# Kernel tuning notes

Measured on AMD Instinct MI355X. Metric: run time of the kernel, lower is better.

The kernel has to match this reference:

```python
import jax, jax.numpy as jnp
import numpy as np

ND, NL, E, M = 8000, 16000, 60000, 50000  # disease nodes, lncrna nodes, edges, label edges
H = 16  # attention heads


def _gat(h_src, h_dst, src, dst, Ws, Wd, a_s, a_d, b, n_dst):
    # PyG GATConv: bipartite, concat heads, add_self_loops=False, negative_slope=0.2
    Hh, C = a_s.shape
    zs = (h_src @ Ws).reshape(-1, Hh, C)   # [Ns,H,C]
    zd = (h_dst @ Wd).reshape(-1, Hh, C)   # [Nd,H,C]
    al = (zs * a_s).sum(-1)[src] + (zd * a_d).sum(-1)[dst]  # [E,H]
    al = jax.nn.leaky_relu(al, negative_slope=0.2)
    m = jax.ops.segment_max(al, dst, num_segments=n_dst)
    m = jnp.where(jnp.isfinite(m), m, 0.0)  # guard empty segments
    e = jnp.exp(al - m[dst])
    s = jax.ops.segment_sum(e, dst, num_segments=n_dst)
    alpha = e / (s[dst] + 1e-16)            # softmax over incoming edges per dst
    msg = zs[src] * alpha[:, :, None]       # [E,H,C]
    out = jax.ops.segment_sum(msg, dst, num_segments=n_dst)
    return out.reshape(n_dst, Hh * C) + b


def _head_mean(x):
    x = jax.nn.relu(x)
    return x.reshape(x.shape[0], H, -1).mean(axis=1)


def _forward(x_d, x_l, emb_d, emb_l, lin_dw, lin_db, lin_lw, lin_lb,
             Wsrc1, Wdst1, asrc1, adst1, b1,
             Wsrc2, Wdst2, asrc2, adst2, b2,
             Wsrc3, Wdst3, asrc3, adst3, b3,
             pw, pb, fc1w, fc1b, fc2w, fc2b,
             node_id_d, node_id_l, edge_src, edge_dst, label_src, label_dst):
    hd = x_d @ lin_dw + lin_db + emb_d[node_id_d]   # [ND,128]
    hl = x_l @ lin_lw + lin_lb + emb_l[node_id_l]   # [NL,128]
    for (Ws, Wd, a_s, a_d, b) in ((Wsrc1, Wdst1, asrc1, adst1, b1),
                                  (Wsrc2, Wdst2, asrc2, adst2, b2),
                                  (Wsrc3, Wdst3, asrc3, adst3, b3)):
        # to_hetero: edge-type 0 = disease->lncrna (target lncrna); 1 = reverse
        out_l = _gat(hd, hl, edge_src, edge_dst, Ws[0], Wd[0], a_s[0], a_d[0], b[0], NL)
        out_d = _gat(hl, hd, edge_dst, edge_src, Ws[1], Wd[1], a_s[1], a_d[1], b[1], ND)
        hd, hl = _head_mean(out_d), _head_mean(out_l)
    # penalty scaling (per node type after to_hetero); transformer branch is dead code
    hd = hd * jnp.exp(hd @ pw[0] + pb[0])
    hl = hl * jnp.exp(hl @ pw[1] + pb[1])
    f = jnp.concatenate([hd[label_src], hl[label_dst]], axis=-1)  # [M,64]
    return jax.nn.relu(f @ fc1w + fc1b) @ fc2w + fc2b              # [M,1]


def setup_inputs():
    key = jax.random.key(0)
    ks = jax.random.split(key, 40)
    def rn(i, shape, scale=1.0):
        return jax.random.normal(ks[i], shape, dtype=jnp.float32) * scale
    return dict(
        x_d=rn(0, (ND, 412)), x_l=rn(1, (NL, 240)),
        node_id_d=jnp.arange(ND), node_id_l=jnp.arange(NL),
        edge_src=jax.random.randint(ks[2], (E,), 0, ND),
        edge_dst=jax.random.randint(ks[3], (E,), 0, NL),
        label_src=jax.random.randint(ks[4], (M,), 0, ND),
        label_dst=jax.random.randint(ks[5], (M,), 0, NL),
        emb_d=rn(6, (ND, 128), 0.1), emb_l=rn(7, (NL, 128), 0.1),
        lin_dw=rn(8, (412, 128), 412 ** -0.5), lin_db=rn(9, (128,), 0.02),
        lin_lw=rn(10, (240, 128), 240 ** -0.5), lin_lb=rn(11, (128,), 0.02),
        Wsrc1=rn(12, (2, 128, 2048), 128 ** -0.5), Wdst1=rn(13, (2, 128, 2048), 128 ** -0.5),
        asrc1=rn(14, (2, H, 128), 0.05), adst1=rn(15, (2, H, 128), 0.05), b1=rn(16, (2, 2048), 0.02),
        Wsrc2=rn(17, (2, 128, 2048), 128 ** -0.5), Wdst2=rn(18, (2, 128, 2048), 128 ** -0.5),
        asrc2=rn(19, (2, H, 128), 0.05), adst2=rn(20, (2, H, 128), 0.05), b2=rn(21, (2, 2048), 0.02),
        Wsrc3=rn(22, (2, 128, 512), 128 ** -0.5), Wdst3=rn(23, (2, 128, 512), 128 ** -0.5),
        asrc3=rn(24, (2, H, 32), 0.05), adst3=rn(25, (2, H, 32), 0.05), b3=rn(26, (2, 512), 0.02),
        pw=rn(27, (2, 32, 1), 0.05), pb=rn(28, (2, 1), 0.01),
        fc1w=rn(29, (64, 64), 64 ** -0.5), fc1b=rn(30, (64,), 0.02),
        fc2w=rn(31, (64, 1), 64 ** -0.5), fc2b=rn(32, (1,), 0.02),
    )


def reference(x_d, x_l, node_id_d, node_id_l, edge_src, edge_dst, label_src, label_dst,
              emb_d, emb_l, lin_dw, lin_db, lin_lw, lin_lb,
              Wsrc1, Wdst1, asrc1, adst1, b1,
              Wsrc2, Wdst2, asrc2, adst2, b2,
              Wsrc3, Wdst3, asrc3, adst3, b3,
              pw, pb, fc1w, fc1b, fc2w, fc2b):
    return _forward(x_d, x_l, emb_d, emb_l, lin_dw, lin_db, lin_lw, lin_lb,
                    Wsrc1, Wdst1, asrc1, adst1, b1,
                    Wsrc2, Wdst2, asrc2, adst2, b2,
                    Wsrc3, Wdst3, asrc3, adst3, b3,
                    pw, pb, fc1w, fc1b, fc2w, fc2b,
                    node_id_d, node_id_l, edge_src, edge_dst, label_src, label_dst)
```

## Files before the change

kernel.cpp:

```cpp
#include <hip/hip_runtime.h>
#include <cstdint>
#include <cstddef>

#define ND 8000
#define NL 16000
#define NE 60000
#define NM 50000

#define BM 64
#define BN 64
#define BK 16

typedef __attribute__((ext_vector_type(8))) short bf16x8;
typedef __attribute__((ext_vector_type(4))) float f32x4;
typedef __attribute__((ext_vector_type(8))) unsigned int u32x8;

__device__ __forceinline__ unsigned short f2bf(float x) {
    unsigned int u = __float_as_uint(x);
    unsigned int r = (u + 0x7FFFu + ((u >> 16) & 1u)) >> 16;
    return (unsigned short)r;
}
__device__ __forceinline__ float bf2f(unsigned short b) {
    return __uint_as_float(((unsigned int)b) << 16);
}
__device__ __forceinline__ float lrelu(float x) {
    return x >= 0.f ? x : 0.2f * x;
}

__device__ __forceinline__ void gl_lds16(const void* g, void* l) {
    __builtin_amdgcn_global_load_lds(
        (const __attribute__((address_space(1))) void*)g,
        (__attribute__((address_space(3))) void*)l, 16, 0, 0);
}

__global__ __launch_bounds__(256) void inlin_kernel(
    const float* __restrict__ x_d, const float* __restrict__ x_l,
    const float* __restrict__ wd, const float* __restrict__ wl,
    const float* __restrict__ bd, const float* __restrict__ bl,
    const float* __restrict__ embd, const float* __restrict__ embl,
    const int* __restrict__ nidd, const int* __restrict__ nidl,
    float* __restrict__ hd, float* __restrict__ hl)
{
    __shared__ float As[BK][32 + 4];
    __shared__ float Bs[BK][BN + 4];
    int mt = blockIdx.y;
    const float* A; const float* B; const float* bias; const float* emb;
    const int* nid; float* out;
    int K;
    if (mt < 250) {
        A = x_d; B = wd; bias = bd; emb = embd; nid = nidd; out = hd; K = 412;
    } else {
        mt -= 250;
        A = x_l; B = wl; bias = bl; emb = embl; nid = nidl; out = hl; K = 240;
    }
    const int tid = threadIdx.x;
    const int tx = tid & 15, ty = tid >> 4;
    const int bm = mt * 32, bn = blockIdx.x * BN;

    const int aml0 = tid >> 4, akl0 = tid & 15;
    const int aml1 = (tid + 256) >> 4, akl1 = tid & 15;
    const int bkl = tid >> 6, bnl = tid & 63;

    float pa[2], pb[4];
    {
        int gk0 = akl0, gk1 = akl1;
        pa[0] = (gk0 < K) ? A[(size_t)(bm + aml0) * K + gk0] : 0.f;
        pa[1] = (gk1 < K) ? A[(size_t)(bm + aml1) * K + gk1] : 0.f;
#pragma unroll
        for (int i = 0; i < 4; ++i) {
            int gk = bkl + i * 4;
            pb[i] = (gk < K) ? B[(size_t)gk * 128 + bn + bnl] : 0.f;
        }
    }

    float acc[2][4] = {};
    for (int k0 = 0; k0 < K; k0 += BK) {
        As[akl0][aml0] = pa[0];
        As[akl1][aml1] = pa[1];
#pragma unroll
        for (int i = 0; i < 4; ++i)
            Bs[bkl + i * 4][bnl] = pb[i];
        __syncthreads();
        int kn = k0 + BK;
        if (kn < K) {
            int gk0 = kn + akl0, gk1 = kn + akl1;
            pa[0] = (gk0 < K) ? A[(size_t)(bm + aml0) * K + gk0] : 0.f;
            pa[1] = (gk1 < K) ? A[(size_t)(bm + aml1) * K + gk1] : 0.f;
#pragma unroll
            for (int i = 0; i < 4; ++i) {
                int gk = kn + bkl + i * 4;
                pb[i] = (gk < K) ? B[(size_t)gk * 128 + bn + bnl] : 0.f;
            }
        }
#pragma unroll
        for (int k = 0; k < BK; ++k) {
            float a0 = As[k][ty * 2];
            float a1 = As[k][ty * 2 + 1];
            float4 bv = *(const float4*)&Bs[k][tx * 4];
            float b4[4] = {bv.x, bv.y, bv.z, bv.w};
#pragma unroll
            for (int j = 0; j < 4; ++j) {
                acc[0][j] += a0 * b4[j];
                acc[1][j] += a1 * b4[j];
            }
        }
        __syncthreads();
    }
#pragma unroll
    for (int i = 0; i < 2; ++i) {
        int gm = bm + ty * 2 + i;
        int gn0 = bn + tx * 4;
        const float* ep = emb + (size_t)nid[gm] * 128 + gn0;
        float4 v;
        float* vp = &v.x;
#pragma unroll
        for (int j = 0; j < 4; ++j)
            vp[j] = acc[i][j] + bias[gn0 + j] + ep[j];
        *(float4*)&out[(size_t)gm * 128 + gn0] = v;
    }
}

__global__ void wt2_kernel(const float* __restrict__ W0, const float* __restrict__ W1,
                           unsigned short* __restrict__ WtH, unsigned short* __restrict__ WtL)
{
    int gid = blockIdx.x * 256 + threadIdx.x;
    if (gid >= 2 * 2 * 128 * 2048) return;
    int l = gid >> 19;
    int rem0 = gid & 524287;
    int dir = rem0 >> 18;
    int rem = rem0 & 262143;
    int k = rem >> 11, n = rem & 2047;
    const float* W = l ? W1 : W0;
    float v = W[(size_t)dir * 262144 + (size_t)k * 2048 + n];
    unsigned short hb = f2bf(v);
    unsigned short lb = f2bf(v - bf2f(hb));
    int u = n >> 4;
    int lane = (n & 15) + 16 * ((k >> 3) & 3);
    size_t o = (size_t)l * 524288 + (size_t)dir * 262144 +
               ((size_t)u * 4 + (k >> 5)) * 512 + lane * 8 + (k & 7);
    WtH[o] = hb;
    WtL[o] = lb;
}

__global__ void wt3_kernel(const float* __restrict__ W3,
                           unsigned short* __restrict__ WtH3, unsigned short* __restrict__ WtL3)
{
    int gid = blockIdx.x * 256 + threadIdx.x;
    if (gid >= 2 * 128 * 512) return;
    int dir = gid >> 16;
    int rem = gid & 65535;
    int k = rem >> 9, n = rem & 511;
    float v = W3[(size_t)dir * 65536 + (size_t)k * 512 + n];
    unsigned short hb = f2bf(v);
    unsigned short lb = f2bf(v - bf2f(hb));
    int u = n >> 4;
    int lane = (n & 15) + 16 * ((k >> 3) & 3);
    size_t o = (size_t)dir * 65536 + ((size_t)u * 4 + (k >> 5)) * 512 + lane * 8 + (k & 7);
    WtH3[o] = hb;
    WtL3[o] = lb;
}

__global__ void pack3_kernel(const float* __restrict__ hd, const float* __restrict__ hl,
                             unsigned int* __restrict__ pAd, unsigned int* __restrict__ pAl)
{
    int gid = blockIdx.x * 256 + threadIdx.x;
    if (gid >= (ND + NL) * 128) return;
    int row = gid >> 7, k = gid & 127;
    const float* src; unsigned int* dst; int gm;
    if (row < ND) { src = hd; dst = pAd; gm = row; }
    else { src = hl; dst = pAl; gm = row - ND; }
    float v = src[(size_t)gm * 128 + k];
    unsigned short hb = f2bf(v);
    unsigned short lb = f2bf(v - bf2f(hb));
    int t = gm >> 4;
    int lane8 = ((gm & 15) + 16 * ((k >> 3) & 3)) * 8 + (k & 7);
    size_t idx = ((size_t)t * 4 + (k >> 5)) * 512 + lane8;
    dst[idx] = (unsigned int)hb | ((unsigned int)lb << 16);
}

__global__ __launch_bounds__(256) void gemm3m_kernel(
    const unsigned int* __restrict__ pAd, const unsigned int* __restrict__ pAl,
    const unsigned short* __restrict__ WtH3, const unsigned short* __restrict__ WtL3,
    float* __restrict__ zs3d, float* __restrict__ zs3l)
{
    const int tid = threadIdx.x;
    const int wave = tid >> 6;
    const int lane = tid & 63;
    const int cb = blockIdx.x & 1;
    int mt = blockIdx.x >> 1;
    const unsigned int* pA_; const unsigned short* wH; const unsigned short* wL; float* zs;
    if (mt < 125) { pA_ = pAd; wH = WtH3; wL = WtL3; zs = zs3d; }
    else { mt -= 125; pA_ = pAl; wH = WtH3 + 65536; wL = WtL3 + 65536; zs = zs3l; }
    const int m0 = mt * 64 + wave * 16;
    const int t = m0 >> 4;
    const int row = lane & 15;
    const int quad = lane >> 4;

    bf16x8 aH[4], aL[4];
#pragma unroll
    for (int kc = 0; kc < 4; ++kc) {
        u32x8 p = *(const u32x8*)(pA_ + ((size_t)t * 4 + kc) * 512 + lane * 8);
#pragma unroll
        for (int ii = 0; ii < 8; ++ii) {
            aH[kc][ii] = (short)(p[ii] & 0xffffu);
            aL[kc][ii] = (short)(p[ii] >> 16);
        }
    }

#pragma unroll 2
    for (int u = 0; u < 16; ++u) {
        const int ug = cb * 16 + u;
        f32x4 accH = (f32x4){0.f, 0.f, 0.f, 0.f};
        f32x4 accL = (f32x4){0.f, 0.f, 0.f, 0.f};
#pragma unroll
        for (int kc = 0; kc < 4; ++kc) {
            size_t boff = ((size_t)ug * 4 + kc) * 512 + lane * 8;
            bf16x8 bH = *(const bf16x8*)(wH + boff);
            bf16x8 bL = *(const bf16x8*)(wL + boff);
            accH = __builtin_amdgcn_mfma_f32_16x16x32_bf16(aH[kc], bH, accH, 0, 0, 0);
            accL = __builtin_amdgcn_mfma_f32_16x16x32_bf16(aH[kc], bL, accL, 0, 0, 0);
            accL = __builtin_amdgcn_mfma_f32_16x16x32_bf16(aL[kc], bH, accL, 0, 0, 0);
        }
        const int gn = ug * 16 + row;
#pragma unroll
        for (int r = 0; r < 4; ++r) {
            int gm = m0 + quad * 4 + r;
            zs[(size_t)gm * 512 + gn] = accH[r] + accL[r];
        }
    }
}

__global__ __launch_bounds__(256) void gemm2r_kernel(
    const unsigned int* __restrict__ haggP,
    const unsigned short* __restrict__ WtH, const unsigned short* __restrict__ WtL,
    const float* __restrict__ bias, float* __restrict__ out, int M)
{
    __shared__ unsigned short BsH[2][8192];
    __shared__ unsigned short BsL[2][8192];

    const int tid = threadIdx.x;
    const int wave = tid >> 6;
    const int lane = tid & 63;
    const int i = blockIdx.x;
    const int cb = i & 1;
    const int mt = i >> 1;
    const int m0 = mt * 64 + wave * 16;
    const int t = m0 >> 4;
    const int row = lane & 15;
    const int quad = lane >> 4;

    const unsigned short* gHb = WtH + (size_t)cb * 8192;
    const unsigned short* gLb = WtL + (size_t)cb * 8192;

    u32x8 pA[4];

    f32x4 mean[4] = {};

#pragma unroll
    for (int j = 0; j < 4; ++j) {
        int o = (tid + j * 256) * 16;
        gl_lds16((const char*)gHb + o, (char*)&BsH[0][0] + o);
        gl_lds16((const char*)gLb + o, (char*)&BsL[0][0] + o);
    }
#pragma unroll
    for (int kc = 0; kc < 4; ++kc)
        pA[kc] = *(const u32x8*)(haggP + (((size_t)t * 16 + 0) * 4 + kc) * 512 + lane * 8);
    __syncthreads();

    int buf = 0;
    for (int h = 0; h < 16; ++h) {
        bf16x8 aH[4], aL[4];
#pragma unroll
        for (int kc = 0; kc < 4; ++kc) {
#pragma unroll
            for (int ii = 0; ii < 8; ++ii) {
                aH[kc][ii] = (short)(pA[kc][ii] & 0xffffu);
                aL[kc][ii] = (short)(pA[kc][ii] >> 16);
            }
        }
        if (h < 15) {
            const char* gH = (const char*)(gHb + (size_t)(h + 1) * 16384);
            const char* gL = (const char*)(gLb + (size_t)(h + 1) * 16384);
            char* lH = (char*)&BsH[buf ^ 1][0];
            char* lL = (char*)&BsL[buf ^ 1][0];
#pragma unroll
            for (int j = 0; j < 4; ++j) {
                int o = (tid + j * 256) * 16;
                gl_lds16(gH + o, lH + o);
                gl_lds16(gL + o, lL + o);
            }
#pragma unroll
            for (int kc = 0; kc < 4; ++kc)
                pA[kc] = *(const u32x8*)(haggP + (((size_t)t * 16 + h + 1) * 4 + kc) * 512 + lane * 8);
        }

#pragma unroll
        for (int ctl = 0; ctl < 4; ++ctl) {
            float bv = bias[h * 128 + cb * 64 + ctl * 16 + row];
            f32x4 accH = (f32x4){bv, bv, bv, bv};
            f32x4 accL = (f32x4){0.f, 0.f, 0.f, 0.f};
#pragma unroll
            for (int kc = 0; kc < 4; ++kc) {
                bf16x8 bH = *(const bf16x8*)&BsH[buf][(ctl * 4 + kc) * 512 + lane * 8];
                bf16x8 bL = *(const bf16x8*)&BsL[buf][(ctl * 4 + kc) * 512 + lane * 8];
                accH = __builtin_amdgcn_mfma_f32_16x16x32_bf16(aH[kc], bH, accH, 0, 0, 0);
                accL = __builtin_amdgcn_mfma_f32_16x16x32_bf16(aH[kc], bL, accL, 0, 0, 0);
                accL = __builtin_amdgcn_mfma_f32_16x16x32_bf16(aL[kc], bH, accL, 0, 0, 0);
            }
#pragma unroll
            for (int r = 0; r < 4; ++r)
                mean[ctl][r] += fmaxf(accH[r] + accL[r], 0.f);
        }
        __syncthreads();
        buf ^= 1;
    }

#pragma unroll
    for (int ctl = 0; ctl < 4; ++ctl) {
        int c = cb * 64 + ctl * 16 + row;
#pragma unroll
        for (int r = 0; r < 4; ++r) {
            int gm = m0 + quad * 4 + r;
            out[(size_t)gm * 128 + c] = mean[ctl][r] * (1.f / 16.f);
        }
    }
}

__global__ void fold3_kernel(
    const float* __restrict__ Ws1, const float* __restrict__ Wd1,
    const float* __restrict__ as1, const float* __restrict__ ad1,
    const float* __restrict__ Ws2, const float* __restrict__ Wd2,
    const float* __restrict__ as2, const float* __restrict__ ad2,
    const float* __restrict__ Ws3, const float* __restrict__ Wd3,
    const float* __restrict__ as3, const float* __restrict__ ad3,
    float* __restrict__ fw3)
{
    int gid = blockIdx.x * blockDim.x + threadIdx.x;
    if (gid >= 3 * 4 * 128 * 16) return;
    int l = gid / 8192, rem1 = gid % 8192;
    int f = rem1 / 2048, rem = rem1 % 2048;
    int k = rem >> 4, h = rem & 15;
    int Ntot = (l == 2) ? 512 : 2048;
    int C = Ntot >> 4;
    const float* W;
    const float* a;
    if (l == 0) { W = (f & 1) ? Wd1 : Ws1; a = (f & 1) ? ad1 : as1; }
    else if (l == 1) { W = (f & 1) ? Wd2 : Ws2; a = (f & 1) ? ad2 : as2; }
    else { W = (f & 1) ? Wd3 : Ws3; a = (f & 1) ? ad3 : as3; }
    if (f >= 2) { W += 128 * Ntot; a += 16 * C; }
    float s = 0.f;
    for (int c = 0; c < C; ++c) s += W[(size_t)k * Ntot + h * C + c] * a[h * C + c];
    fw3[gid] = s;
}

__global__ __launch_bounds__(256) void score2both_kernel(
    const float* __restrict__ Hd, const float* __restrict__ Hl,
    const float* __restrict__ fw,
    float* __restrict__ ssb0, float* __restrict__ sdb1,
    float* __restrict__ sdb0, float* __restrict__ ssb1)
{
    __shared__ float hs[16 * 128];
    __shared__ float wa[128 * 16];
    __shared__ float wb[128 * 16];
    int b = blockIdx.x;
    const float* Hf; const float* WfA; const float* WfB;
    float* outA; float* outB; int n0;
    if (b < ND / 16) {
        Hf = Hd; WfA = fw; WfB = fw + 3 * 2048; outA = ssb0; outB = sdb1; n0 = b * 16;
    } else {
        Hf = Hl; WfA = fw + 1 * 2048; WfB = fw + 2 * 2048; outA = sdb0; outB = ssb1;
        n0 = (b - ND / 16) * 16;
    }
    int tid = threadIdx.x;
#pragma unroll
    for (int i = 0; i < 8; ++i) {
        int idx = tid + i * 256;
        int nl = idx >> 7, k = idx & 127;
        hs[idx] = Hf[(size_t)(n0 + nl) * 128 + k];
        wa[idx] = WfA[idx];
        wb[idx] = WfB[idx];
    }
    __syncthreads();
    int nl = tid >> 4, h = tid & 15;
    float sa = 0.f, sb = 0.f;
    for (int k = 0; k < 128; ++k) {
        float hv = hs[nl * 128 + k];
        sa += hv * wa[k * 16 + h];
        sb += hv * wb[k * 16 + h];
    }
    int gn = n0 + nl;
    outA[gn * 16 + h] = sa;
    outB[gn * 16 + h] = sb;
}

__global__ void ms_kernel(
    const int* __restrict__ esrc, const int* __restrict__ edst,
    const float* __restrict__ ssb0, const float* __restrict__ sdb0,
    const float* __restrict__ ssb1, const float* __restrict__ sdb1,
    const int* __restrict__ offl, const int* __restrict__ csrl, float* __restrict__ msl,
    const int* __restrict__ offd, const int* __restrict__ csrd, float* __restrict__ msd)
{
    int t = blockIdx.x * 256 + threadIdx.x;
    const int* off; const int* csr; const int* srcidx;
    const float* ss; float sdv; float* ms; int d, h;
    if (t < NL * 16) {
        d = t >> 4; h = t & 15;
        off = offl; csr = csrl; srcidx = esrc; ss = ssb0;
        sdv = sdb0[d * 16 + h]; ms = msl;
    } else {
        t -= NL * 16;
        if (t >= ND * 16) return;
        d = t >> 4; h = t & 15;
        off = offd; csr = csrd; srcidx = edst; ss = ssb1;
        sdv = sdb1[d * 16 + h]; ms = msd;
    }
    int e0 = off[d], e1 = off[d + 1];
    float m = -1e30f, s = 0.f;
    for (int e = e0; e < e1; ++e) {
        int sn = srcidx[csr[e]];
        float a = lrelu(ss[sn * 16 + h] + sdv);
        if (a > m) { s = s * __expf(m - a) + 1.f; m = a; }
        else s += __expf(a - m);
    }
    ms[d * 32 + h] = m;
    ms[d * 32 + 16 + h] = s + 1e-16f;
}

__global__ void hist_kernel(const int* __restrict__ esrc, const int* __restrict__ edst,
                            int* __restrict__ degl, int* __restrict__ degd)
{
    int e = blockIdx.x * blockDim.x + threadIdx.x;
    if (e >= NE) return;
    atomicAdd(&degl[edst[e]], 1);
    atomicAdd(&degd[esrc[e]], 1);
}

__global__ __launch_bounds__(1024) void scan2_kernel(
    const int* __restrict__ degA, int* __restrict__ offA, int nA,
    const int* __restrict__ degB, int* __restrict__ offB, int nB)
{
    __shared__ int ps[1024];
    const int* deg = blockIdx.x ? degB : degA;
    int* off = blockIdx.x ? offB : offA;
    int n = blockIdx.x ? nB : nA;
    int tid = threadIdx.x;
    int chunk = (n + 1023) >> 10;
    int start = tid * chunk, end = min(start + chunk, n);
    int p = 0;
    for (int i = start; i < end; ++i) p += deg[i];
    ps[tid] = p;
    __syncthreads();
    for (int o = 1; o < 1024; o <<= 1) {
        int v = (tid >= o) ? ps[tid - o] : 0;
        __syncthreads();
        ps[tid] += v;
        __syncthreads();
    }
    int run = ps[tid] - p;
    for (int i = start; i < end; ++i) { off[i] = run; run += deg[i]; }
    if (tid == 1023) off[n] = ps[1023];
}

__global__ void scatter_kernel(const int* __restrict__ esrc, const int* __restrict__ edst,
                               const int* __restrict__ offl, const int* __restrict__ offd,
                               int* __restrict__ curl, int* __restrict__ curd,
                               int* __restrict__ csrl, int* __restrict__ csrd)
{
    int e = blockIdx.x * blockDim.x + threadIdx.x;
    if (e >= NE) return;
    int dl = edst[e]; int p = atomicAdd(&curl[dl], 1); csrl[offl[dl] + p] = e;
    int dd = esrc[e]; int q = atomicAdd(&curd[dd], 1); csrd[offd[dd] + q] = e;
}

__global__ __launch_bounds__(256) void hagg_kernel(
    const float* __restrict__ hsrc,
    const float* __restrict__ ss,
    const float* __restrict__ sd,
    const float* __restrict__ ms,
    const int* __restrict__ off, const int* __restrict__ csr, const int* __restrict__ srcidx,
    unsigned int* __restrict__ haggP)
{
    __shared__ float alpha_s[2][8][17];
    __shared__ int src_s[2][8];
    const int d0 = blockIdx.x * 2;
    const int tid = threadIdx.x;

    const int half = tid >> 7;
    const int c = tid & 127;
    const int d = d0 + half;
    const int my_e0 = off[d];
    const int my_deg = off[d + 1] - my_e0;
    const int deg0 = off[d0 + 1] - off[d0];
    const int deg1 = off[d0 + 2] - off[d0 + 1];
    const int degmax = deg0 > deg1 ? deg0 : deg1;
    const int ntrip = (degmax + 7) >> 3;

    float acc[16];
#pragma unroll
    for (int h = 0; h < 16; ++h) acc[h] = 0.f;

    for (int trip = 0; trip < ntrip; ++trip) {
        int ce = trip * 8;
        {
            int ei = c >> 4, h = c & 15;
            if (ce + ei < my_deg) {
                int eid = csr[my_e0 + ce + ei];
                int sn = srcidx[eid];
                float a = lrelu(ss[sn * 16 + h] + sd[d * 16 + h]);
                alpha_s[half][ei][h] = __expf(a - ms[d * 32 + h]) / ms[d * 32 + 16 + h];
                if (h == 0) src_s[half][ei] = sn;
            }
        }
        __syncthreads();
        int nc = min(8, my_deg - ce);
        for (int ei = 0; ei < nc; ++ei) {
            float v = hsrc[(size_t)src_s[half][ei] * 128 + c];
#pragma unroll
            for (int h = 0; h < 16; ++h)
                acc[h] += alpha_s[half][ei][h] * v;
        }
        __syncthreads();
    }

    const int t = d >> 4;
    const int lane8 = ((d & 15) + 16 * ((c >> 3) & 3)) * 8 + (c & 7);
    const int kc = c >> 5;
#pragma unroll
    for (int h = 0; h < 16; ++h) {
        float v = acc[h];
        unsigned short hb = f2bf(v);
        unsigned short lb = f2bf(v - bf2f(hb));
        size_t idx = (((size_t)t * 16 + h) * 4 + kc) * 512 + lane8;
        haggP[idx] = (unsigned int)hb | ((unsigned int)lb << 16);
    }
}

__global__ __launch_bounds__(256) void agg32both_kernel(
    const float* __restrict__ zs3d, const float* __restrict__ zs3l,
    const float* __restrict__ ssb0, const float* __restrict__ sdb0, const float* __restrict__ msl,
    const float* __restrict__ ssb1, const float* __restrict__ sdb1, const float* __restrict__ msd,
    const int* __restrict__ offl, const int* __restrict__ csrl,
    const int* __restrict__ offd, const int* __restrict__ csrd,
    const int* __restrict__ esrc, const int* __restrict__ edst,
    const float* __restrict__ bias512,
    const float* __restrict__ pw, const float* __restrict__ pb,
    float* __restrict__ hlp, float* __restrict__ hdp)
{
    int d = blockIdx.x * 4 + (threadIdx.x >> 6);
    if (d >= NL + ND) return;
    const int lane = threadIdx.x & 63;

    const float* zs; const float* ss; const float* sd; const float* ms;
    const int* off; const int* csr; const int* srcidx;
    const float* bias; const float* pwt; const float* pbt; float* out;
    if (d < NL) {
        zs = zs3d; ss = ssb0; sd = sdb0; ms = msl;
        off = offl; csr = csrl; srcidx = esrc;
        bias = bias512; pwt = pw + 32; pbt = pb + 1; out = hlp;
    } else {
        d -= NL;
        zs = zs3l; ss = ssb1; sd = sdb1; ms = msd;
        off = offd; csr = csrd; srcidx = edst;
        bias = bias512 + 512; pwt = pw; pbt = pb; out = hdp;
    }

    const int h = lane >> 2;
    const int c0 = lane * 8;

    const float sdv = sd[d * 16 + h];
    const float mh = ms[d * 32 + h];
    const float sh = ms[d * 32 + 16 + h];
    const int e0 = off[d], e1 = off[d + 1];

    float acc[8] = {};
    for (int e = e0; e < e1; ++e) {
        int sn = srcidx[csr[e]];
        float a = lrelu(ss[sn * 16 + h] + sdv);
        float alpha = __expf(a - mh) / sh;
        const float* zr = zs + (size_t)sn * 512 + c0;
        float4 v0 = *(const float4*)zr;
        float4 v1 = *(const float4*)(zr + 4);
        acc[0] += alpha * v0.x; acc[1] += alpha * v0.y;
        acc[2] += alpha * v0.z; acc[3] += alpha * v0.w;
        acc[4] += alpha * v1.x; acc[5] += alpha * v1.y;
        acc[6] += alpha * v1.z; acc[7] += alpha * v1.w;
    }

#pragma unroll
    for (int i = 0; i < 8; ++i)
        acc[i] = fmaxf(acc[i] + bias[c0 + i], 0.f);

#pragma unroll
    for (int m = 4; m <= 32; m <<= 1)
#pragma unroll
        for (int i = 0; i < 8; ++i)
            acc[i] += __shfl_xor(acc[i], m);

    float hr[8];
#pragma unroll
    for (int i = 0; i < 8; ++i) hr[i] = acc[i] * (1.f / 16.f);

    float p = 0.f;
    const int ko = (lane & 3) * 8;
#pragma unroll
    for (int i = 0; i < 8; ++i) p += hr[i] * pwt[ko + i];
    p += __shfl_xor(p, 1);
    p += __shfl_xor(p, 2);
    float t = expf(p + pbt[0]);

    if (lane < 4) {
        float* op = out + (size_t)d * 32 + lane * 8;
#pragma unroll
        for (int i = 0; i < 8; ++i) op[i] = hr[i] * t;
    }
}

__global__ __launch_bounds__(256) void mlp_kernel(
    const float* __restrict__ hd, const float* __restrict__ hl,
    const int* __restrict__ ls, const int* __restrict__ ld,
    const float* __restrict__ w1, const float* __restrict__ b1,
    const float* __restrict__ w2, const float* __restrict__ b2,
    float* __restrict__ out, int M)
{
    __shared__ float w1s[64 * 64];
    __shared__ float b1s[64];
    __shared__ float w2s[64];
    int tid = threadIdx.x;
#pragma unroll
    for (int i = 0; i < 16; ++i) w1s[tid + i * 256] = w1[tid + i * 256];
    if (tid < 64) { b1s[tid] = b1[tid]; w2s[tid] = w2[tid]; }
    __syncthreads();
    int m = blockIdx.x * 256 + tid;
    if (m >= M) return;
    float f[64];
    const float* hp = hd + (size_t)ls[m] * 32;
    const float* lp = hl + (size_t)ld[m] * 32;
#pragma unroll
    for (int c = 0; c < 32; ++c) { f[c] = hp[c]; f[32 + c] = lp[c]; }
    float o = b2[0];
    for (int j = 0; j < 64; ++j) {
        float hj = b1s[j];
#pragma unroll
        for (int k = 0; k < 64; ++k) hj += f[k] * w1s[k * 64 + j];
        hj = fmaxf(hj, 0.f);
        o += hj * w2s[j];
    }
    out[m] = o;
}

extern "C" void kernel_launch(void* const* d_in, const int* in_sizes, int n_in,
                              void* d_out, int out_size, void* d_ws, size_t ws_size,
                              hipStream_t stream)
{
    const float* x_d = (const float*)d_in[0];
    const float* x_l = (const float*)d_in[1];
    const int* node_id_d = (const int*)d_in[2];
    const int* node_id_l = (const int*)d_in[3];
    const int* edge_src = (const int*)d_in[4];
    const int* edge_dst = (const int*)d_in[5];
    const int* label_src = (const int*)d_in[6];
    const int* label_dst = (const int*)d_in[7];
    const float* emb_d = (const float*)d_in[8];
    const float* emb_l = (const float*)d_in[9];
    const float* lin_dw = (const float*)d_in[10];
    const float* lin_db = (const float*)d_in[11];
    const float* lin_lw = (const float*)d_in[12];
    const float* lin_lb = (const float*)d_in[13];
    const float* Ws[3] = {(const float*)d_in[14], (const float*)d_in[19], (const float*)d_in[24]};
    const float* Wd[3] = {(const float*)d_in[15], (const float*)d_in[20], (const float*)d_in[25]};
    const float* as_[3] = {(const float*)d_in[16], (const float*)d_in[21], (const float*)d_in[26]};
    const float* ad_[3] = {(const float*)d_in[17], (const float*)d_in[22], (const float*)d_in[27]};
    const float* bb[3] = {(const float*)d_in[18], (const float*)d_in[23], (const float*)d_in[28]};
    const float* pw = (const float*)d_in[29];
    const float* pb = (const float*)d_in[30];
    const float* fc1w = (const float*)d_in[31];
    const float* fc1b = (const float*)d_in[32];
    const float* fc2w = (const float*)d_in[33];
    const float* fc2b = (const float*)d_in[34];

    char* wsb = (char*)d_ws;
    size_t woff = 0;
    auto carve = [&](size_t bytes) -> void* {
        woff = (woff + 255) & ~(size_t)255;
        void* p = wsb + woff;
        woff += bytes;
        return p;
    };
    float* hdA = (float*)carve((size_t)ND * 128 * 4);
    float* hlA = (float*)carve((size_t)NL * 128 * 4);
    float* hdB = (float*)carve((size_t)ND * 128 * 4);
    float* hlB = (float*)carve((size_t)NL * 128 * 4);
    unsigned int* haggP = (unsigned int*)carve((size_t)NL * 2048 * 4);
    unsigned short* WtH = (unsigned short*)carve((size_t)2 * 2 * 2048 * 128 * 2);
    unsigned short* WtL = (unsigned short*)carve((size_t)2 * 2 * 2048 * 128 * 2);
    unsigned short* WtH3 = (unsigned short*)carve((size_t)2 * 128 * 512 * 2);
    unsigned short* WtL3 = (unsigned short*)carve((size_t)2 * 128 * 512 * 2);
    unsigned int* pAd = (unsigned int*)carve((size_t)(ND / 16) * 4 * 512 * 4);
    unsigned int* pAl = (unsigned int*)carve((size_t)(NL / 16) * 4 * 512 * 4);
    float* ssb0 = (float*)carve((size_t)ND * 16 * 4);
    float* sdb0 = (float*)carve((size_t)NL * 16 * 4);
    float* ssb1 = (float*)carve((size_t)NL * 16 * 4);
    float* sdb1 = (float*)carve((size_t)ND * 16 * 4);
    float* msl = (float*)carve((size_t)NL * 32 * 4);
    float* msd = (float*)carve((size_t)ND * 32 * 4);
    float* fw3 = (float*)carve((size_t)3 * 4 * 2048 * 4);
    int* degl = (int*)carve((size_t)(2 * (NL + ND)) * 4);
    int* degd = degl + NL;
    int* curl = degd + ND;
    int* curd = curl + NL;
    int* offl = (int*)carve((size_t)(NL + 1) * 4);
    int* offd = (int*)carve((size_t)(ND + 1) * 4);
    int* csrl = (int*)carve((size_t)NE * 4);
    int* csrd = (int*)carve((size_t)NE * 4);
    float* hdp = (float*)carve((size_t)ND * 32 * 4);
    float* hlp = (float*)carve((size_t)NL * 32 * 4);

    hipMemsetAsync(degl, 0, (size_t)2 * (NL + ND) * 4, stream);

    hist_kernel<<<(NE + 255) / 256, 256, 0, stream>>>(edge_src, edge_dst, degl, degd);
    scan2_kernel<<<2, 1024, 0, stream>>>(degl, offl, NL, degd, offd, ND);
    scatter_kernel<<<(NE + 255) / 256, 256, 0, stream>>>(edge_src, edge_dst, offl, offd, curl, curd, csrl, csrd);

    fold3_kernel<<<(3 * 8192 + 255) / 256, 256, 0, stream>>>(
        Ws[0], Wd[0], as_[0], ad_[0], Ws[1], Wd[1], as_[1], ad_[1],
        Ws[2], Wd[2], as_[2], ad_[2], fw3);
    wt2_kernel<<<(2 * 524288 + 255) / 256, 256, 0, stream>>>(Ws[0], Ws[1], WtH, WtL);
    wt3_kernel<<<(2 * 65536 + 255) / 256, 256, 0, stream>>>(Ws[2], WtH3, WtL3);

    inlin_kernel<<<dim3(2, 750), 256, 0, stream>>>(
        x_d, x_l, lin_dw, lin_lw, lin_db, lin_lb, emb_d, emb_l,
        node_id_d, node_id_l, hdA, hlA);

    float* hd_cur = hdA; float* hd_nxt = hdB;
    float* hl_cur = hlA; float* hl_nxt = hlB;

    const int grid_ms = ((NL + ND) * 16 + 255) / 256;
    const int gridNL = (NL / 64) * 2;
    const int gridND = (ND / 64) * 2;

    for (int L = 0; L < 2; ++L) {
        const float* fw = fw3 + (size_t)L * 8192;
        const unsigned short* wtH = WtH + (size_t)L * 524288;
        const unsigned short* wtL = WtL + (size_t)L * 524288;

        score2both_kernel<<<ND / 16 + NL / 16, 256, 0, stream>>>(
            hd_cur, hl_cur, fw, ssb0, sdb1, sdb0, ssb1);
        ms_kernel<<<grid_ms, 256, 0, stream>>>(edge_src, edge_dst, ssb0, sdb0, ssb1, sdb1,
                                               offl, csrl, msl, offd, csrd, msd);

        hagg_kernel<<<NL / 2, 256, 0, stream>>>(hd_cur, ssb0, sdb0, msl, offl, csrl, edge_src, haggP);
        gemm2r_kernel<<<gridNL, 256, 0, stream>>>(haggP, wtH, wtL, bb[L], hl_nxt, NL);

        hagg_kernel<<<ND / 2, 256, 0, stream>>>(hl_cur, ssb1, sdb1, msd, offd, csrd, edge_dst, haggP);
        gemm2r_kernel<<<gridND, 256, 0, stream>>>(haggP,
                                                  wtH + (size_t)2048 * 128, wtL + (size_t)2048 * 128,
                                                  bb[L] + 2048, hd_nxt, ND);

        float* t;
        t = hd_cur; hd_cur = hd_nxt; hd_nxt = t;
        t = hl_cur; hl_cur = hl_nxt; hl_nxt = t;
    }

    {
        const float* fw = fw3 + 2 * 8192;
        float* zs3d = (float*)haggP;
        float* zs3l = (float*)haggP + (size_t)ND * 512;
        score2both_kernel<<<ND / 16 + NL / 16, 256, 0, stream>>>(
            hd_cur, hl_cur, fw, ssb0, sdb1, sdb0, ssb1);
        ms_kernel<<<grid_ms, 256, 0, stream>>>(edge_src, edge_dst, ssb0, sdb0, ssb1, sdb1,
                                               offl, csrl, msl, offd, csrd, msd);

        pack3_kernel<<<((ND + NL) * 128 + 255) / 256, 256, 0, stream>>>(
            hd_cur, hl_cur, pAd, pAl);
        gemm3m_kernel<<<(125 + 250) * 2, 256, 0, stream>>>(
            pAd, pAl, WtH3, WtL3, zs3d, zs3l);

        agg32both_kernel<<<(NL + ND) / 4, 256, 0, stream>>>(
            zs3d, zs3l, ssb0, sdb0, msl, ssb1, sdb1, msd,
            offl, csrl, offd, csrd, edge_src, edge_dst,
            bb[2], pw, pb, hlp, hdp);
    }

    mlp_kernel<<<(NM + 255) / 256, 256, 0, stream>>>(hdp, hlp, label_src, label_dst,
                                                     fc1w, fc1b, fc2w, fc2b, (float*)d_out, NM);
}
```

Before: 679.1 us.

## Move input linear layer to split-bf16 MFMA and quarter gemm2r column tiles

Replaces the FP32 SIMT tiled input projection with an MFMA kernel that uses three bf16 products (hi*hi, hi*lo, lo*hi) to keep near-fp32 accuracy. A new weight packing kernel prepares the hi/lo bf16 fragments in MFMA lane layout. Separately, gemm2r now splits output columns into four blocks per row tile instead of two, halving LDS per block to raise the block count and occupancy. The cost is redundant A-fragment loads across more blocks and one extra small pre-pass kernel.

```diff
diff --git a/kernel.cpp b/kernel.cpp
--- a/kernel.cpp
+++ b/kernel.cpp
@@ -7,10 +7,6 @@
 #define NE 60000
 #define NM 50000
 
-#define BM 64
-#define BN 64
-#define BK 16
-
 typedef __attribute__((ext_vector_type(8))) short bf16x8;
 typedef __attribute__((ext_vector_type(4))) float f32x4;
 typedef __attribute__((ext_vector_type(8))) unsigned int u32x8;
@@ -33,90 +29,100 @@
         (__attribute__((address_space(3))) void*)l, 16, 0, 0);
 }
 
-__global__ __launch_bounds__(256) void inlin_kernel(
+__global__ void wtin_kernel(const float* __restrict__ Wd, const float* __restrict__ Wl,
+                            unsigned short* __restrict__ WinH, unsigned short* __restrict__ WinL)
+{
+    int gid = blockIdx.x * 256 + threadIdx.x;
+    if (gid >= 53248 + 32768) return;
+    const float* W; int K, KC; unsigned short* oH; unsigned short* oL; int rem;
+    if (gid < 53248) { W = Wd; K = 412; KC = 13; rem = gid; oH = WinH; oL = WinL; }
+    else { W = Wl; K = 240; KC = 8; rem = gid - 53248; oH = WinH + 53248; oL = WinL + 53248; }
+    int k = rem >> 7, n = rem & 127;
+    float v = (k < K) ? W[(size_t)k * 128 + n] : 0.f;
+    unsigned short hb = f2bf(v);
+    unsigned short lb = f2bf(v - bf2f(hb));
+    int u = n >> 4;
+    int kc = k >> 5;
+    int lane = (n & 15) + 16 * ((k >> 3) & 3);
+    size_t o = ((size_t)u * KC + kc) * 512 + lane * 8 + (k & 7);
+    oH[o] = hb;
+    oL[o] = lb;
+}
+
+__global__ __launch_bounds__(256) void inlinm_kernel(
     const float* __restrict__ x_d, const float* __restrict__ x_l,
-    const float* __restrict__ wd, const float* __restrict__ wl,
+    const unsigned short* __restrict__ WinH, const unsigned short* __restrict__ WinL,
     const float* __restrict__ bd, const float* __restrict__ bl,
     const float* __restrict__ embd, const float* __restrict__ embl,
     const int* __restrict__ nidd, const int* __restrict__ nidl,
     float* __restrict__ hd, float* __restrict__ hl)
 {
-    __shared__ float As[BK][32 + 4];
-    __shared__ float Bs[BK][BN + 4];
-    int mt = blockIdx.y;
-    const float* A; const float* B; const float* bias; const float* emb;
-    const int* nid; float* out;
-    int K;
-    if (mt < 250) {
-        A = x_d; B = wd; bias = bd; emb = embd; nid = nidd; out = hd; K = 412;
+    const int tid = threadIdx.x;
+    const int wave = tid >> 6;
+    const int lane = tid & 63;
+    const int i = blockIdx.x;
+    const int cb = i & 1;
+    int mt = i >> 1;
+    const float* X; int K, KC;
+    const unsigned short* wH; const unsigned short* wL;
+    const float* bias; const float* emb; const int* nid; float* out;
+    if (mt < 125) {
+        X = x_d; K = 412; KC = 13; wH = WinH; wL = WinL;
+        bias = bd; emb = embd; nid = nidd; out = hd;
     } else {
-        mt -= 250;
-        A = x_l; B = wl; bias = bl; emb = embl; nid = nidl; out = hl; K = 240;
-    }
-    const int tid = threadIdx.x;
-    const int tx = tid & 15, ty = tid >> 4;
-    const int bm = mt * 32, bn = blockIdx.x * BN;
-
-    const int aml0 = tid >> 4, akl0 = tid & 15;
-    const int aml1 = (tid + 256) >> 4, akl1 = tid & 15;
-    const int bkl = tid >> 6, bnl = tid & 63;
-
-    float pa[2], pb[4];
-    {
-        int gk0 = akl0, gk1 = akl1;
-        pa[0] = (gk0 < K) ? A[(size_t)(bm + aml0) * K + gk0] : 0.f;
-        pa[1] = (gk1 < K) ? A[(size_t)(bm + aml1) * K + gk1] : 0.f;
-#pragma unroll
-        for (int i = 0; i < 4; ++i) {
-            int gk = bkl + i * 4;
-            pb[i] = (gk < K) ? B[(size_t)gk * 128 + bn + bnl] : 0.f;
-        }
-    }
-
-    float acc[2][4] = {};
-    for (int k0 = 0; k0 < K; k0 += BK) {
-        As[akl0][aml0] = pa[0];
-        As[akl1][aml1] = pa[1];
-#pragma unroll
-        for (int i = 0; i < 4; ++i)
-            Bs[bkl + i * 4][bnl] = pb[i];
-        __syncthreads();
-        int kn = k0 + BK;
-        if (kn < K) {
-            int gk0 = kn + akl0, gk1 = kn + akl1;
-            pa[0] = (gk0 < K) ? A[(size_t)(bm + aml0) * K + gk0] : 0.f;
-            pa[1] = (gk1 < K) ? A[(size_t)(bm + aml1) * K + gk1] : 0.f;
-#pragma unroll
-            for (int i = 0; i < 4; ++i) {
-                int gk = kn + bkl + i * 4;
-                pb[i] = (gk < K) ? B[(size_t)gk * 128 + bn + bnl] : 0.f;
-            }
-        }
-#pragma unroll
-        for (int k = 0; k < BK; ++k) {
-            float a0 = As[k][ty * 2];
-            float a1 = As[k][ty * 2 + 1];
-            float4 bv = *(const float4*)&Bs[k][tx * 4];
-            float b4[4] = {bv.x, bv.y, bv.z, bv.w};
-#pragma unroll
-            for (int j = 0; j < 4; ++j) {
-                acc[0][j] += a0 * b4[j];
-                acc[1][j] += a1 * b4[j];
-            }
-        }
-        __syncthreads();
-    }
-#pragma unroll
-    for (int i = 0; i < 2; ++i) {
-        int gm = bm + ty * 2 + i;
-        int gn0 = bn + tx * 4;
-        const float* ep = emb + (size_t)nid[gm] * 128 + gn0;
-        float4 v;
-        float* vp = &v.x;
-#pragma unroll
-        for (int j = 0; j < 4; ++j)
-            vp[j] = acc[i][j] + bias[gn0 + j] + ep[j];
-        *(float4*)&out[(size_t)gm * 128 + gn0] = v;
+        mt -= 125;
+        X = x_l; K = 240; KC = 8; wH = WinH + 53248; wL = WinL + 53248;
+        bias = bl; emb = embl; nid = nidl; out = hl;
+    }
+    const int m0 = mt * 64 + wave * 16;
+    const int row = lane & 15;
+    const int quad = lane >> 4;
+
+    f32x4 accH[4] = {};
+    f32x4 accL[4] = {};
+
+    const float* xr = X + (size_t)(m0 + row) * K;
+    for (int kc = 0; kc < KC; ++kc) {
+        int k0 = kc * 32 + quad * 8;
+        float xv[8];
+        if (k0 + 8 <= K) {
+            float4 v0 = *(const float4*)(xr + k0);
+            float4 v1 = *(const float4*)(xr + k0 + 4);
+            xv[0] = v0.x; xv[1] = v0.y; xv[2] = v0.z; xv[3] = v0.w;
+            xv[4] = v1.x; xv[5] = v1.y; xv[6] = v1.z; xv[7] = v1.w;
+        } else {
+#pragma unroll
+            for (int j = 0; j < 8; ++j)
+                xv[j] = (k0 + j < K) ? xr[k0 + j] : 0.f;
+        }
+        bf16x8 aH, aL;
+#pragma unroll
+        for (int j = 0; j < 8; ++j) {
+            unsigned short hb = f2bf(xv[j]);
+            aH[j] = (short)hb;
+            aL[j] = (short)f2bf(xv[j] - bf2f(hb));
+        }
+#pragma unroll
+        for (int u = 0; u < 4; ++u) {
+            int ug = cb * 4 + u;
+            size_t boff = ((size_t)ug * KC + kc) * 512 + lane * 8;
+            bf16x8 bH = *(const bf16x8*)(wH + boff);
+            bf16x8 bL = *(const bf16x8*)(wL + boff);
+            accH[u] = __builtin_amdgcn_mfma_f32_16x16x32_bf16(aH, bH, accH[u], 0, 0, 0);
+            accL[u] = __builtin_amdgcn_mfma_f32_16x16x32_bf16(aH, bL, accL[u], 0, 0, 0);
+            accL[u] = __builtin_amdgcn_mfma_f32_16x16x32_bf16(aL, bH, accL[u], 0, 0, 0);
+        }
+    }
+#pragma unroll
+    for (int r = 0; r < 4; ++r) {
+        int gm = m0 + quad * 4 + r;
+        const float* ep = emb + (size_t)nid[gm] * 128;
+        float* op = out + (size_t)gm * 128;
+#pragma unroll
+        for (int u = 0; u < 4; ++u) {
+            int gn = (cb * 4 + u) * 16 + row;
+            op[gn] = accH[u][r] + accL[u][r] + bias[gn] + ep[gn];
+        }
     }
 }
 
@@ -235,29 +241,28 @@
     const unsigned short* __restrict__ WtH, const unsigned short* __restrict__ WtL,
     const float* __restrict__ bias, float* __restrict__ out, int M)
 {
-    __shared__ unsigned short BsH[2][8192];
-    __shared__ unsigned short BsL[2][8192];
+    __shared__ unsigned short BsH[2][4096];
+    __shared__ unsigned short BsL[2][4096];
 
     const int tid = threadIdx.x;
     const int wave = tid >> 6;
     const int lane = tid & 63;
     const int i = blockIdx.x;
-    const int cb = i & 1;
-    const int mt = i >> 1;
+    const int cb = i & 3;
+    const int mt = i >> 2;
     const int m0 = mt * 64 + wave * 16;
     const int t = m0 >> 4;
     const int row = lane & 15;
     const int quad = lane >> 4;
 
-    const unsigned short* gHb = WtH + (size_t)cb * 8192;
-    const unsigned short* gLb = WtL + (size_t)cb * 8192;
+    const unsigned short* gHb = WtH + (size_t)cb * 4096;
+    const unsigned short* gLb = WtL + (size_t)cb * 4096;
 
     u32x8 pA[4];
-
-    f32x4 mean[4] = {};
-
-#pragma unroll
-    for (int j = 0; j < 4; ++j) {
+    f32x4 mean[2] = {};
+
+#pragma unroll
+    for (int j = 0; j < 2; ++j) {
         int o = (tid + j * 256) * 16;
         gl_lds16((const char*)gHb + o, (char*)&BsH[0][0] + o);
         gl_lds16((const char*)gLb + o, (char*)&BsL[0][0] + o);
@@ -284,7 +289,7 @@
             char* lH = (char*)&BsH[buf ^ 1][0];
             char* lL = (char*)&BsL[buf ^ 1][0];
 #pragma unroll
-            for (int j = 0; j < 4; ++j) {
+            for (int j = 0; j < 2; ++j) {
                 int o = (tid + j * 256) * 16;
                 gl_lds16(gH + o, lH + o);
                 gl_lds16(gL + o, lL + o);
@@ -295,8 +300,8 @@
         }
 
 #pragma unroll
-        for (int ctl = 0; ctl < 4; ++ctl) {
-            float bv = bias[h * 128 + cb * 64 + ctl * 16 + row];
+        for (int ctl = 0; ctl < 2; ++ctl) {
+            float bv = bias[h * 128 + cb * 32 + ctl * 16 + row];
             f32x4 accH = (f32x4){bv, bv, bv, bv};
             f32x4 accL = (f32x4){0.f, 0.f, 0.f, 0.f};
 #pragma unroll
@@ -316,8 +321,8 @@
     }
 
 #pragma unroll
-    for (int ctl = 0; ctl < 4; ++ctl) {
-        int c = cb * 64 + ctl * 16 + row;
+    for (int ctl = 0; ctl < 2; ++ctl) {
+        int c = cb * 32 + ctl * 16 + row;
 #pragma unroll
         for (int r = 0; r < 4; ++r) {
             int gm = m0 + quad * 4 + r;
@@ -695,6 +700,8 @@
     unsigned short* WtL = (unsigned short*)carve((size_t)2 * 2 * 2048 * 128 * 2);
     unsigned short* WtH3 = (unsigned short*)carve((size_t)2 * 128 * 512 * 2);
     unsigned short* WtL3 = (unsigned short*)carve((size_t)2 * 128 * 512 * 2);
+    unsigned short* WtInH = (unsigned short*)carve((size_t)(53248 + 32768) * 2);
+    unsigned short* WtInL = (unsigned short*)carve((size_t)(53248 + 32768) * 2);
     unsigned int* pAd = (unsigned int*)carve((size_t)(ND / 16) * 4 * 512 * 4);
     unsigned int* pAl = (unsigned int*)carve((size_t)(NL / 16) * 4 * 512 * 4);
     float* ssb0 = (float*)carve((size_t)ND * 16 * 4);
@@ -726,17 +733,18 @@
         Ws[2], Wd[2], as_[2], ad_[2], fw3);
     wt2_kernel<<<(2 * 524288 + 255) / 256, 256, 0, stream>>>(Ws[0], Ws[1], WtH, WtL);
     wt3_kernel<<<(2 * 65536 + 255) / 256, 256, 0, stream>>>(Ws[2], WtH3, WtL3);
-
-    inlin_kernel<<<dim3(2, 750), 256, 0, stream>>>(
-        x_d, x_l, lin_dw, lin_lw, lin_db, lin_lb, emb_d, emb_l,
+    wtin_kernel<<<(53248 + 32768 + 255) / 256, 256, 0, stream>>>(lin_dw, lin_lw, WtInH, WtInL);
+
+    inlinm_kernel<<<(125 + 250) * 2, 256, 0, stream>>>(
+        x_d, x_l, WtInH, WtInL, lin_db, lin_lb, emb_d, emb_l,
         node_id_d, node_id_l, hdA, hlA);
 
     float* hd_cur = hdA; float* hd_nxt = hdB;
     float* hl_cur = hlA; float* hl_nxt = hlB;
 
     const int grid_ms = ((NL + ND) * 16 + 255) / 256;
-    const int gridNL = (NL / 64) * 2;
-    const int gridND = (ND / 64) * 2;
+    const int gridNL = (NL / 64) * 4;
+    const int gridND = (ND / 64) * 4;
 
     for (int L = 0; L < 2; ++L) {
         const float* fw = fw3 + (size_t)L * 8192;
@@ -775,7 +783,7 @@
         gemm3m_kernel<<<(125 + 250) * 2, 256, 0, stream>>>(
             pAd, pAl, WtH3, WtL3, zs3d, zs3l);
 
-        agg32both_kernel<<<(NL + ND) / 4, 256, 0, stream>>>(
+        agg32both_kernel<<<(NL + ND + 3) / 4, 256, 0, stream>>>(
             zs3d, zs3l, ssb0, sdb0, msl, ssb1, sdb1, msd,
             offl, csrl, offd, csrd, edge_src, edge_dst,
             bb[2], pw, pb, hlp, hdp);
```

After: 749.7 us. 10.4% more time.
